# Kernel tuning notes

Hardware: AMD Instinct MI355X
Metric: run time of the kernel (lower is better)

Reference implementation:

```python
import jax, jax.numpy as jnp
import numpy as np

H = 8  # num_heads
EPS = 1e-6


def _pos_encoding(S, D):
    # absolute sinusoidal positional encoding, shape [S, D]
    pos = jnp.arange(S, dtype=jnp.float32)[:, None]
    div = jnp.exp(jnp.arange(0, D, 2, dtype=jnp.float32) * (-np.log(10000.0) / D))
    pe = jnp.zeros((S, D), dtype=jnp.float32)
    pe = pe.at[:, 0::2].set(jnp.sin(pos * div))
    pe = pe.at[:, 1::2].set(jnp.cos(pos * div))
    return pe


def setup_inputs() -> dict:
    key = jax.random.key(0)
    ks = jax.random.split(key, 5)
    S, B, D = 2048, 16, 1024
    s = 1.0 / np.sqrt(D)
    return {
        'x': jax.random.normal(ks[0], (S, B, D), dtype=jnp.float32),
        'Wq': jax.random.normal(ks[1], (D, D), dtype=jnp.float32) * s,
        'bq': jnp.zeros((D,), dtype=jnp.float32),
        'Wk': jax.random.normal(ks[2], (D, D), dtype=jnp.float32) * s,
        'bk': jnp.zeros((D,), dtype=jnp.float32),
        'Wv': jax.random.normal(ks[3], (D, D), dtype=jnp.float32) * s,
        'bv': jnp.zeros((D,), dtype=jnp.float32),
        'Wo': jax.random.normal(ks[4], (D, D), dtype=jnp.float32) * s,
        'bo': jnp.zeros((D,), dtype=jnp.float32),
    }


def reference(x, Wq, bq, Wk, bk, Wv, bv, Wo, bo):
    # x: [S, B, D]  (nn.Transformer layout)
    S, B, D = x.shape
    dh = D // H
    h = x + _pos_encoding(S, D)[:, None, :]
    # projections (torch Linear: y = x @ W.T + b), split into heads
    q = (h @ Wq.T + bq).reshape(S, B, H, dh)
    k = (h @ Wk.T + bk).reshape(S, B, H, dh)
    v = (h @ Wv.T + bv).reshape(S, B, H, dh)
    # kernel feature map phi(u) = elu(u) + 1 (Katharopoulos linear attention)
    pq = jax.nn.elu(q) + 1.0
    pk = jax.nn.elu(k) + 1.0
    # global (non-causal) linear attention:
    # kv state: sum_s phi(k_s) v_s^T  -> [B, H, dh, dh]
    kv = jnp.einsum('sbhd,sbhe->bhde', pk, v)
    # normalizer: sum_s phi(k_s)     -> [B, H, dh]
    z = pk.sum(axis=0)
    num = jnp.einsum('sbhd,bhde->sbhe', pq, kv)   # [S, B, H, dh]
    den = jnp.einsum('sbhd,bhd->sbh', pq, z)       # [S, B, H]
    att = num / (den[..., None] + EPS)
    out = att.reshape(S, B, D) @ Wo.T + bo
    return out
```

## Files before the change

kernel.cpp:

```cpp
#include <hip/hip_runtime.h>
#include <hip/hip_bf16.h>
#include <stdint.h>


typedef __bf16 bf16x8 __attribute__((ext_vector_type(8)));
typedef float f32x4 __attribute__((ext_vector_type(4)));

#define S_LEN 2048
#define B_SZ  16
#define D_MOD 1024
#define N_H   8
#define D_H   128

__device__ __forceinline__ short f2bf(float f) {
  __bf16 b = (__bf16)f;
  return __builtin_bit_cast(short, b);
}
__device__ __forceinline__ float bf2f(short s) {
  return (float)__builtin_bit_cast(__bf16, s);
}

__device__ __forceinline__ void gload_lds16(const short* g, short* l) {
  __builtin_amdgcn_global_load_lds(
      (__attribute__((address_space(1))) void*)(g),
      (__attribute__((address_space(3))) void*)(l), 16, 0, 0);
}

__device__ __forceinline__ int swz(int o) { return o ^ (((o >> 7) & 3) << 4); }

__device__ __forceinline__ bf16x8 ld_bf8_8al(const short* p) {
  union { unsigned long long u[2]; bf16x8 v; } x;
  x.u[0] = *(const unsigned long long*)p;
  x.u[1] = *(const unsigned long long*)(p + 4);
  return x.v;
}

__global__ void prep_h(const float* __restrict__ x, short* __restrict__ h) {
  size_t idx8 = (size_t)blockIdx.x * blockDim.x + threadIdx.x;
  size_t base = idx8 * 8;
  int d = (int)(base & 1023);
  int r = (int)(base >> 10);
  int s = r >> 4;
  float4 v0 = *(const float4*)(x + base);
  float4 v1 = *(const float4*)(x + base + 4);
  float vs[8] = {v0.x, v0.y, v0.z, v0.w, v1.x, v1.y, v1.z, v1.w};
  const float kdiv = -9.210340371976184f / 1024.0f;
  bf16x8 ov;
#pragma unroll
  for (int t = 0; t < 8; ++t) {
    int dc = d + t;
    float div = __expf((float)(dc & ~1) * kdiv);
    float ang = (float)s * div;
    float pe = (dc & 1) ? __cosf(ang) : __sinf(ang);
    ov[t] = (__bf16)(vs[t] + pe);
  }
  *(bf16x8*)(h + base) = ov;
}

__global__ void pack_w(const float* __restrict__ Wq, const float* __restrict__ Wk,
                       const float* __restrict__ Wv, const float* __restrict__ Wo,
                       short* __restrict__ Wcat) {
  size_t i4 = (size_t)blockIdx.x * blockDim.x + threadIdx.x;
  size_t base = i4 * 4;
  const float* src;
  size_t off;
  if (base < 1048576)      { src = Wq; off = base; }
  else if (base < 2097152) { src = Wk; off = base - 1048576; }
  else if (base < 3145728) { src = Wv; off = base - 2097152; }
  else                     { src = Wo; off = base - 3145728; }
  float4 v = *(const float4*)(src + off);
  alignas(8) short o[4] = {f2bf(v.x), f2bf(v.y), f2bf(v.z), f2bf(v.w)};
  *(uint2*)(Wcat + base) = *(const uint2*)o;
}

template <int K>
__device__ __forceinline__ void core_256(const short* __restrict__ A,
                                         const short* __restrict__ W,
                                         char* Lb, f32x4 (&acc)[8][4]) {
  constexpr int NT = K / 32;
  static_assert(NT >= 4, "pipeline needs K >= 128");
  const int tid = threadIdx.x;
  const int lane = tid & 63;
  const int wave = tid >> 6;
  const int wm = wave & 1, wn = wave >> 1;
  const int l15 = lane & 15, quad = lane >> 4;

  const int oA0 = tid * 16, oA1 = 8192 + tid * 16;
  const int lA0 = swz(oA0), lA1 = swz(oA1);
  const short* gA0 = A + (size_t)(lA0 >> 6) * K + ((lA0 & 63) >> 1);
  const short* gA1 = A + (size_t)((lA1 - 8192) >> 6) * K + 128 * K + (((lA1 - 8192) & 63) >> 1);
  const short* gW0 = W + (size_t)(lA0 >> 6) * K + ((lA0 & 63) >> 1);
  const short* gW1 = W + (size_t)((lA1 - 8192) >> 6) * K + 128 * K + (((lA1 - 8192) & 63) >> 1);

  int rA[8], rW[4];
#pragma unroll
  for (int i = 0; i < 8; ++i)
    rA[i] = swz((wm * 128 + i * 16 + l15) * 64 + quad * 16);
#pragma unroll
  for (int j = 0; j < 4; ++j)
    rW[j] = 16384 + swz((wn * 64 + j * 16 + l15) * 64 + quad * 16);

  auto stage = [&](int t) {
    char* sb = Lb + (t & 3) * 32768;
    const int k0 = t * 32;
    gload_lds16(gA0 + k0, (short*)(sb + oA0));
    gload_lds16(gA1 + k0, (short*)(sb + oA1));
    gload_lds16(gW0 + k0, (short*)(sb + 16384 + oA0));
    gload_lds16(gW1 + k0, (short*)(sb + 16384 + oA1));
  };
  auto step = [&](int t, bool do_stage) {
    char* cb = Lb + (t & 3) * 32768;
    bf16x8 af[8], wf[4];
#pragma unroll
    for (int i = 0; i < 8; ++i) af[i] = *(const bf16x8*)(cb + rA[i]);
#pragma unroll
    for (int j = 0; j < 4; ++j) wf[j] = *(const bf16x8*)(cb + rW[j]);
    if (do_stage) stage(t + 3);
    __builtin_amdgcn_s_setprio(1);
#pragma unroll
    for (int i = 0; i < 8; ++i)
#pragma unroll
      for (int j = 0; j < 4; ++j)
        acc[i][j] = __builtin_amdgcn_mfma_f32_16x16x32_bf16(af[i], wf[j], acc[i][j], 0, 0, 0);
    __builtin_amdgcn_s_setprio(0);
    asm volatile("s_waitcnt lgkmcnt(0)" ::: "memory");
    __builtin_amdgcn_sched_barrier(0);
  };

  stage(0); stage(1); stage(2);

  for (int t = 0; t <= NT - 4; ++t) {
    asm volatile("s_waitcnt vmcnt(8)" ::: "memory");
    __builtin_amdgcn_s_barrier();
    step(t, true);
  }
  asm volatile("s_waitcnt vmcnt(8)" ::: "memory");
  __builtin_amdgcn_s_barrier();
  step(NT - 3, false);
  asm volatile("s_waitcnt vmcnt(4)" ::: "memory");
  __builtin_amdgcn_s_barrier();
  step(NT - 2, false);
  asm volatile("s_waitcnt vmcnt(0)" ::: "memory");
  __builtin_amdgcn_s_barrier();
  step(NT - 1, false);
}

template <int K>
__device__ __forceinline__ void core_128(const short* __restrict__ A,
                                         const short* __restrict__ W,
                                         char* Lb, f32x4 (&acc)[4][4]) {
  constexpr int NT = K / 32;
  static_assert(NT >= 4, "pipeline needs K >= 128");
  const int tid = threadIdx.x;
  const int lane = tid & 63;
  const int wm = (tid >> 6) & 1, wn = tid >> 7;
  const int l15 = lane & 15, quad = lane >> 4;

  const int oA0 = tid * 16, oA1 = 4096 + tid * 16;
  const int lA0 = swz(oA0), lA1 = swz(oA1);
  const short* gA0 = A + (size_t)(lA0 >> 6) * K + ((lA0 & 63) >> 1);
  const short* gA1 = A + (size_t)((lA1 - 4096) >> 6) * K + 64 * K + (((lA1 - 4096) & 63) >> 1);
  const short* gW0 = W + (size_t)(lA0 >> 6) * K + ((lA0 & 63) >> 1);
  const short* gW1 = W + (size_t)((lA1 - 4096) >> 6) * K + 64 * K + (((lA1 - 4096) & 63) >> 1);

  int rA[4], rW[4];
#pragma unroll
  for (int i = 0; i < 4; ++i)
    rA[i] = swz((wm * 64 + i * 16 + l15) * 64 + quad * 16);
#pragma unroll
  for (int j = 0; j < 4; ++j)
    rW[j] = 8192 + swz((wn * 64 + j * 16 + l15) * 64 + quad * 16);

  auto stage = [&](int t) {
    char* sb = Lb + (t & 3) * 16384;
    const int k0 = t * 32;
    gload_lds16(gA0 + k0, (short*)(sb + oA0));
    gload_lds16(gA1 + k0, (short*)(sb + oA1));
    gload_lds16(gW0 + k0, (short*)(sb + 8192 + oA0));
    gload_lds16(gW1 + k0, (short*)(sb + 8192 + oA1));
  };
  auto step = [&](int t, bool do_stage) {
    char* cb = Lb + (t & 3) * 16384;
    bf16x8 af[4], wf[4];
#pragma unroll
    for (int i = 0; i < 4; ++i) af[i] = *(const bf16x8*)(cb + rA[i]);
#pragma unroll
    for (int j = 0; j < 4; ++j) wf[j] = *(const bf16x8*)(cb + rW[j]);
    if (do_stage) stage(t + 3);
    __builtin_amdgcn_s_setprio(1);
#pragma unroll
    for (int i = 0; i < 4; ++i)
#pragma unroll
      for (int j = 0; j < 4; ++j)
        acc[i][j] = __builtin_amdgcn_mfma_f32_16x16x32_bf16(af[i], wf[j], acc[i][j], 0, 0, 0);
    __builtin_amdgcn_s_setprio(0);
    asm volatile("s_waitcnt lgkmcnt(0)" ::: "memory");
    __builtin_amdgcn_sched_barrier(0);
  };

  stage(0); stage(1); stage(2);

  for (int t = 0; t <= NT - 4; ++t) {
    asm volatile("s_waitcnt vmcnt(8)" ::: "memory");
    __builtin_amdgcn_s_barrier();
    step(t, true);
  }
  asm volatile("s_waitcnt vmcnt(8)" ::: "memory");
  __builtin_amdgcn_s_barrier();
  step(NT - 3, false);
  asm volatile("s_waitcnt vmcnt(4)" ::: "memory");
  __builtin_amdgcn_s_barrier();
  step(NT - 2, false);
  asm volatile("s_waitcnt vmcnt(0)" ::: "memory");
  __builtin_amdgcn_s_barrier();
  step(NT - 1, false);
}

__launch_bounds__(512, 2)
__global__ void gemm_qkv(const short* __restrict__ h, const short* __restrict__ Wqkv,
                         const float* __restrict__ bq, const float* __restrict__ bk,
                         const float* __restrict__ bv,
                         short* __restrict__ pq, short* __restrict__ pk,
                         short* __restrict__ pv) {
  __shared__ alignas(16) char Lb[131072];
  const int lin = blockIdx.y * 12 + blockIdx.x;
  const int x = lin & 7, q = lin >> 3;
  const int xm = x >> 1, xn = x & 1;
  const int bm = xm * 32 + q / 6;
  const int bn = xn * 6 + q % 6;
  const int rowBase = bm * 256, colBase = bn * 256;

  f32x4 acc[8][4] = {};
  core_256<1024>(h + (size_t)rowBase * 1024, Wqkv + (size_t)colBase * 1024, Lb, acc);

  const int tid = threadIdx.x;
  const int lane = tid & 63;
  const int wave = tid >> 6;
  const int wm = wave & 1, wn = wave >> 1;
  const int l15 = lane & 15, quad = lane >> 4;

  const int p = bn >> 2;
  const float* bias = (p == 0) ? bq : (p == 1) ? bk : bv;
  short* Pout = (p == 0) ? pq : (p == 1) ? pk : pv;

  __syncthreads();
  short* Lt = (short*)Lb;
#pragma unroll
  for (int j = 0; j < 4; ++j) {
    const int c = wn * 64 + j * 16 + l15;
    const float bval = bias[(bn & 3) * 256 + c];
#pragma unroll
    for (int i = 0; i < 8; ++i) {
#pragma unroll
      for (int r = 0; r < 4; ++r) {
        const int mloc = wm * 128 + i * 16 + quad * 4 + r;
        float v = acc[i][j][r] + bval;
        if (p < 2) v = v > 0.f ? v + 1.f : __expf(v);
        Lt[mloc * 256 + (c ^ ((mloc & 7) << 3))] = f2bf(v);
      }
    }
  }
  __syncthreads();
  const int g16 = tid >> 4, L = tid & 15;
#pragma unroll
  for (int it = 0; it < 16; ++it) {
    const int chunk = it * 32 + g16;
    const int row = chunk >> 1, hhl = chunk & 1;
    const int grow = rowBase + row;
    const int s = grow >> 4, b = grow & 15;
    const int hh = (bn & 3) * 2 + hhl;
    const short* src = Lt + row * 256 + ((hhl * 128 + L * 8) ^ ((row & 7) << 3));
    short* dst = Pout + (((size_t)b * N_H + hh) * S_LEN + s) * D_H + L * 8;
    *(uint4*)dst = *(const uint4*)src;
  }
}

__launch_bounds__(256, 2)
__global__ void kv_kernel(const short* __restrict__ pk, const short* __restrict__ pv,
                          short* __restrict__ kvT, float* __restrict__ z) {
  __shared__ alignas(16) short Vt[128 * 44];
  __shared__ alignas(16) short Pt[128 * 44];
  __shared__ float zl[16 * 128];
  const int bh = blockIdx.x;
  const short* Vg = pv + (size_t)bh * S_LEN * D_H;
  const short* Pg = pk + (size_t)bh * S_LEN * D_H;

  const int tid = threadIdx.x;
  const int lane = tid & 63;
  const int wm = (tid >> 6) & 1, wn = tid >> 7;
  const int l15 = lane & 15, quad = lane >> 4;
  const int s_loc = tid >> 3, e8 = tid & 7;

  const short* vsrc = Vg + s_loc * 128 + e8 * 8;
  const short* psrc = Pg + s_loc * 128 + e8 * 8;

  f32x4 acc[4][4] = {};
  uint4 cv0, cv1, cp0, cp1;
  cv0 = *(const uint4*)(vsrc);
  cv1 = *(const uint4*)(vsrc + 64);
  cp0 = *(const uint4*)(psrc);
  cp1 = *(const uint4*)(psrc + 64);

  for (int t = 0; t < 64; ++t) {
    __builtin_amdgcn_s_barrier();
    const short* sv0 = (const short*)&cv0;
    const short* sv1 = (const short*)&cv1;
    const short* sp0 = (const short*)&cp0;
    const short* sp1 = (const short*)&cp1;
#pragma unroll
    for (int u = 0; u < 8; ++u) {
      Vt[(e8 * 8 + u) * 44 + s_loc] = sv0[u];
      Vt[(64 + e8 * 8 + u) * 44 + s_loc] = sv1[u];
      Pt[(e8 * 8 + u) * 44 + s_loc] = sp0[u];
      Pt[(64 + e8 * 8 + u) * 44 + s_loc] = sp1[u];
    }
    if (t < 63) {
      const int o = (t + 1) * 32 * 128;
      cv0 = *(const uint4*)(vsrc + o);
      cv1 = *(const uint4*)(vsrc + o + 64);
      cp0 = *(const uint4*)(psrc + o);
      cp1 = *(const uint4*)(psrc + o + 64);
    }
    asm volatile("s_waitcnt lgkmcnt(0)" ::: "memory");
    __builtin_amdgcn_sched_barrier(0);
    __builtin_amdgcn_s_barrier();
    bf16x8 af[4], wf[4];
#pragma unroll
    for (int i = 0; i < 4; ++i)
      af[i] = ld_bf8_8al(&Vt[(wm * 64 + i * 16 + l15) * 44 + quad * 8]);
#pragma unroll
    for (int j = 0; j < 4; ++j)
      wf[j] = ld_bf8_8al(&Pt[(wn * 64 + j * 16 + l15) * 44 + quad * 8]);
#pragma unroll
    for (int i = 0; i < 4; ++i)
#pragma unroll
      for (int j = 0; j < 4; ++j)
        acc[i][j] = __builtin_amdgcn_mfma_f32_16x16x32_bf16(af[i], wf[j], acc[i][j], 0, 0, 0);
    asm volatile("s_waitcnt lgkmcnt(0)" ::: "memory");
    __builtin_amdgcn_sched_barrier(0);
  }

#pragma unroll
  for (int j = 0; j < 4; ++j) {
    const int d = wn * 64 + j * 16 + l15;
#pragma unroll
    for (int i = 0; i < 4; ++i) {
#pragma unroll
      for (int r = 0; r < 4; ++r) {
        const int e = wm * 64 + i * 16 + quad * 4 + r;
        kvT[(size_t)bh * (D_H * D_H) + (size_t)e * D_H + d] = f2bf(acc[i][j][r]);
      }
    }
  }
  __syncthreads();
  {
    const int d8 = tid & 15, so = tid >> 4;
    float za[8] = {};
    for (int s = so; s < S_LEN; s += 16) {
      uint4 u = *(const uint4*)(Pg + (size_t)s * 128 + d8 * 8);
      const short* sp = (const short*)&u;
#pragma unroll
      for (int u2 = 0; u2 < 8; ++u2) za[u2] += bf2f(sp[u2]);
    }
#pragma unroll
    for (int u2 = 0; u2 < 8; ++u2) zl[so * 128 + d8 * 8 + u2] = za[u2];
  }
  __syncthreads();
  if (tid < 128) {
    float sum = 0.f;
#pragma unroll
    for (int k = 0; k < 16; ++k) sum += zl[k * 128 + tid];
    z[bh * D_H + tid] = sum;
  }
}

__launch_bounds__(256, 2)
__global__ void attn_kernel(const short* __restrict__ pq, const short* __restrict__ kvT,
                            const float* __restrict__ z, short* __restrict__ att) {
  __shared__ alignas(16) char Lb[65536];
  __shared__ float den_lds[128];
  __shared__ float z_lds[128];
  const int s0 = blockIdx.x * 128;
  const int bh = blockIdx.y;
  const int tid = threadIdx.x;

  const short* Abase = pq + ((size_t)bh * S_LEN + s0) * D_H;
  const short* Wbase = kvT + (size_t)bh * (D_H * D_H);

  f32x4 acc[4][4] = {};
  core_128<128>(Abase, Wbase, Lb, acc);

  if (tid < 128) z_lds[tid] = z[bh * D_H + tid];
  __syncthreads();
  if (tid < 128) {
    const short* prow = Abase + (size_t)tid * D_H;
    float sum = 0.f;
#pragma unroll
    for (int d = 0; d < D_H; d += 8) {
      bf16x8 vv = *(const bf16x8*)(prow + d);
#pragma unroll
      for (int t = 0; t < 8; ++t) sum += (float)vv[t] * z_lds[d + t];
    }
    den_lds[tid] = sum + 1e-6f;
  }
  __syncthreads();

  const int lane = tid & 63;
  const int wm = (tid >> 6) & 1, wn = tid >> 7;
  const int l15 = lane & 15, quad = lane >> 4;
  const int b = bh >> 3, hd = bh & 7;
#pragma unroll
  for (int j = 0; j < 4; ++j) {
    const int e = wn * 64 + j * 16 + l15;
#pragma unroll
    for (int i = 0; i < 4; ++i) {
#pragma unroll
      for (int r = 0; r < 4; ++r) {
        int mloc = wm * 64 + i * 16 + quad * 4 + r;
        float a = acc[i][j][r] / den_lds[mloc];
        att[((size_t)(s0 + mloc) * B_SZ + b) * D_MOD + hd * D_H + e] = f2bf(a);
      }
    }
  }
}

__launch_bounds__(512, 2)
__global__ void gemm_out(const short* __restrict__ att, const short* __restrict__ WoB,
                         const float* __restrict__ bo, float* __restrict__ out) {
  __shared__ alignas(16) char Lb[131072];
  const int lin = blockIdx.y * 4 + blockIdx.x;
  const int x = lin & 7, q = lin >> 3;
  const int bn = q & 3;
  const int bm = x * 16 + (q >> 2);
  const int rowBase = bm * 256, colBase = bn * 256;

  f32x4 acc[8][4] = {};
  core_256<1024>(att + (size_t)rowBase * 1024, WoB + (size_t)colBase * 1024, Lb, acc);

  const int tid = threadIdx.x;
  const int lane = tid & 63;
  const int wave = tid >> 6;
  const int wm = wave & 1, wn = wave >> 1;
  const int l15 = lane & 15, quad = lane >> 4;
#pragma unroll
  for (int j = 0; j < 4; ++j) {
    const int gcol = colBase + wn * 64 + j * 16 + l15;
    const float bval = bo[gcol];
#pragma unroll
    for (int i = 0; i < 8; ++i) {
#pragma unroll
      for (int r = 0; r < 4; ++r) {
        int grow = rowBase + wm * 128 + i * 16 + quad * 4 + r;
        out[(size_t)grow * 1024 + gcol] = acc[i][j][r] + bval;
      }
    }
  }
}

extern "C" void kernel_launch(void* const* d_in, const int* in_sizes, int n_in,
                              void* d_out, int out_size, void* d_ws, size_t ws_size,
                              hipStream_t stream) {
  const float* x  = (const float*)d_in[0];
  const float* Wq = (const float*)d_in[1];
  const float* bq = (const float*)d_in[2];
  const float* Wk = (const float*)d_in[3];
  const float* bk = (const float*)d_in[4];
  const float* Wv = (const float*)d_in[5];
  const float* bv = (const float*)d_in[6];
  const float* Wo = (const float*)d_in[7];
  const float* bo = (const float*)d_in[8];
  float* out = (float*)d_out;

  char* ws = (char*)d_ws;
  short* h    = (short*)(ws);
  short* Wcat = (short*)(ws + 67108864);
  short* pq   = (short*)(ws + 75497472);
  short* pk   = (short*)(ws + 142606336);
  short* pv   = (short*)(ws + 209715200);
  short* kvT  = (short*)(ws + 276824064);
  float* z    = (float*)(ws + 281018368);

  prep_h<<<16384, 256, 0, stream>>>(x, h);
  pack_w<<<4096, 256, 0, stream>>>(Wq, Wk, Wv, Wo, Wcat);
  gemm_qkv<<<dim3(12, 128), 512, 0, stream>>>(h, Wcat, bq, bk, bv, pq, pk, pv);
  kv_kernel<<<128, 256, 0, stream>>>(pk, pv, kvT, z);
  attn_kernel<<<dim3(16, 128), 256, 0, stream>>>(pq, kvT, z, h );
  gemm_out<<<dim3(4, 128), 512, 0, stream>>>(h, Wcat + 3145728, bo, out);
}
```

Baseline: 685.6 us.

## Restructure 256-tile GEMM pipeline with K=64 steps and split KV reduction

The 256x256 GEMM core now stages 64-wide K tiles in two LDS buffers, interleaving half-tile LDS reads, async global-to-LDS loads and MFMA groups with barriers between them. The goal is to hide load latency better and keep fewer fragments live in registers. Launch bounds for the two big GEMMs drop to one block per CU to match the full 128KB LDS use. The KV state computation is also split over four sequence chunks with fp32 partials plus a reduce kernel, so 512 blocks run instead of 128. In exchange this adds an extra kernel launch and fp32 partial traffic through the workspace.

After: 637.3 us. 7.0% less time.

```diff
diff --git a/kernel.cpp b/kernel.cpp
--- a/kernel.cpp
+++ b/kernel.cpp
@@ -77,72 +77,97 @@
 __device__ __forceinline__ void core_256(const short* __restrict__ A,
                                          const short* __restrict__ W,
                                          char* Lb, f32x4 (&acc)[8][4]) {
-  constexpr int NT = K / 32;
-  static_assert(NT >= 4, "pipeline needs K >= 128");
+  constexpr int NT = K / 64;
+  static_assert(NT >= 4 && (NT & 1) == 0, "K must be multiple of 128, >= 256");
   const int tid = threadIdx.x;
   const int lane = tid & 63;
   const int wave = tid >> 6;
   const int wm = wave & 1, wn = wave >> 1;
   const int l15 = lane & 15, quad = lane >> 4;
 
-  const int oA0 = tid * 16, oA1 = 8192 + tid * 16;
-  const int lA0 = swz(oA0), lA1 = swz(oA1);
-  const short* gA0 = A + (size_t)(lA0 >> 6) * K + ((lA0 & 63) >> 1);
-  const short* gA1 = A + (size_t)((lA1 - 8192) >> 6) * K + 128 * K + (((lA1 - 8192) & 63) >> 1);
-  const short* gW0 = W + (size_t)(lA0 >> 6) * K + ((lA0 & 63) >> 1);
-  const short* gW1 = W + (size_t)((lA1 - 8192) >> 6) * K + 128 * K + (((lA1 - 8192) & 63) >> 1);
-
-  int rA[8], rW[4];
+  const int o0 = tid * 16, o1 = 8192 + tid * 16;
+  const int r0s = o0 >> 6, r1s = o1 >> 6;
+  const int c0 = ((o0 & 63) ^ (((o0 >> 7) & 3) << 4)) >> 1;
+  const int c1 = ((o1 & 63) ^ (((o1 >> 7) & 3) << 4)) >> 1;
+  const short* gA0 = A + (size_t)r0s * K + c0;
+  const short* gA1 = A + (size_t)r1s * K + c1;
+  const short* gW0 = W + (size_t)r0s * K + c0;
+  const short* gW1 = W + (size_t)r1s * K + c1;
+
+  int rAo[8], rWo[4];
 #pragma unroll
   for (int i = 0; i < 8; ++i)
-    rA[i] = swz((wm * 128 + i * 16 + l15) * 64 + quad * 16);
+    rAo[i] = swz((wm * 128 + i * 16 + l15) * 64 + quad * 16);
 #pragma unroll
   for (int j = 0; j < 4; ++j)
-    rW[j] = 16384 + swz((wn * 64 + j * 16 + l15) * 64 + quad * 16);
-
-  auto stage = [&](int t) {
-    char* sb = Lb + (t & 3) * 32768;
-    const int k0 = t * 32;
-    gload_lds16(gA0 + k0, (short*)(sb + oA0));
-    gload_lds16(gA1 + k0, (short*)(sb + oA1));
-    gload_lds16(gW0 + k0, (short*)(sb + 16384 + oA0));
-    gload_lds16(gW1 + k0, (short*)(sb + 16384 + oA1));
+    rWo[j] = swz((wn * 64 + j * 16 + l15) * 64 + quad * 16);
+
+  bf16x8 af[4], wf[4];
+
+  auto stg = [&](int tau, int op, int kh) {
+    char* d = Lb + (tau & 1) * 65536 + op * 32768 + kh * 16384;
+    const int ko = tau * 64 + kh * 32;
+    const short* s0 = (op ? gW0 : gA0) + ko;
+    const short* s1 = (op ? gW1 : gA1) + ko;
+    gload_lds16(s0, (short*)(d + o0));
+    gload_lds16(s1, (short*)(d + o1));
   };
-  auto step = [&](int t, bool do_stage) {
-    char* cb = Lb + (t & 3) * 32768;
-    bf16x8 af[8], wf[4];
-#pragma unroll
-    for (int i = 0; i < 8; ++i) af[i] = *(const bf16x8*)(cb + rA[i]);
-#pragma unroll
-    for (int j = 0; j < 4; ++j) wf[j] = *(const bf16x8*)(cb + rW[j]);
-    if (do_stage) stage(t + 3);
-    __builtin_amdgcn_s_setprio(1);
-#pragma unroll
-    for (int i = 0; i < 8; ++i)
-#pragma unroll
-      for (int j = 0; j < 4; ++j)
-        acc[i][j] = __builtin_amdgcn_mfma_f32_16x16x32_bf16(af[i], wf[j], acc[i][j], 0, 0, 0);
-    __builtin_amdgcn_s_setprio(0);
+  auto rd0 = [&](int tau, int kh) {
+    char* base = Lb + (tau & 1) * 65536 + kh * 16384;
+#pragma unroll
+    for (int j = 0; j < 4; ++j) wf[j] = *(const bf16x8*)(base + 32768 + rWo[j]);
+#pragma unroll
+    for (int i = 0; i < 4; ++i) af[i] = *(const bf16x8*)(base + rAo[i]);
+  };
+  auto rd1 = [&](int tau, int kh) {
+    char* base = Lb + (tau & 1) * 65536 + kh * 16384;
+#pragma unroll
+    for (int i = 0; i < 4; ++i) af[i] = *(const bf16x8*)(base + rAo[4 + i]);
+  };
+  auto mm = [&](int ih) {
+    __builtin_amdgcn_s_barrier();
     asm volatile("s_waitcnt lgkmcnt(0)" ::: "memory");
     __builtin_amdgcn_sched_barrier(0);
+    __builtin_amdgcn_s_setprio(1);
+#pragma unroll
+    for (int i = 0; i < 4; ++i)
+#pragma unroll
+      for (int j = 0; j < 4; ++j)
+        acc[ih * 4 + i][j] =
+            __builtin_amdgcn_mfma_f32_16x16x32_bf16(af[i], wf[j], acc[ih * 4 + i][j], 0, 0, 0);
+    __builtin_amdgcn_s_setprio(0);
+    __builtin_amdgcn_s_barrier();
   };
 
-  stage(0); stage(1); stage(2);
-
-  for (int t = 0; t <= NT - 4; ++t) {
-    asm volatile("s_waitcnt vmcnt(8)" ::: "memory");
-    __builtin_amdgcn_s_barrier();
-    step(t, true);
-  }
-  asm volatile("s_waitcnt vmcnt(8)" ::: "memory");
+  stg(0, 1, 0); stg(0, 0, 0); stg(0, 1, 1); stg(0, 0, 1);
+  stg(1, 1, 0); stg(1, 0, 0); stg(1, 1, 1);
+  asm volatile("s_waitcnt vmcnt(6)" ::: "memory");
   __builtin_amdgcn_s_barrier();
-  step(NT - 3, false);
-  asm volatile("s_waitcnt vmcnt(4)" ::: "memory");
-  __builtin_amdgcn_s_barrier();
-  step(NT - 2, false);
-  asm volatile("s_waitcnt vmcnt(0)" ::: "memory");
-  __builtin_amdgcn_s_barrier();
-  step(NT - 1, false);
+
+  for (int t = 0; t + 3 < NT; t += 2) {
+    rd0(t, 0);     stg(t + 1, 0, 1);                                          mm(0);
+    rd1(t, 0);     stg(t + 2, 1, 0);                                          mm(1);
+    rd0(t, 1);     stg(t + 2, 0, 0);                                          mm(0);
+    rd1(t, 1);     stg(t + 2, 1, 1);
+    asm volatile("s_waitcnt vmcnt(6)" ::: "memory");                          mm(1);
+    rd0(t + 1, 0); stg(t + 2, 0, 1);                                          mm(0);
+    rd1(t + 1, 0); stg(t + 3, 1, 0);                                          mm(1);
+    rd0(t + 1, 1); stg(t + 3, 0, 0);                                          mm(0);
+    rd1(t + 1, 1); stg(t + 3, 1, 1);
+    asm volatile("s_waitcnt vmcnt(6)" ::: "memory");                          mm(1);
+  }
+  {
+    const int t = NT - 2;
+    rd0(t, 0);     stg(t + 1, 0, 1);                                          mm(0);
+    rd1(t, 0);                                                                mm(1);
+    rd0(t, 1);                                                                mm(0);
+    rd1(t, 1);
+    asm volatile("s_waitcnt vmcnt(0)" ::: "memory");                          mm(1);
+    rd0(t + 1, 0);                                                            mm(0);
+    rd1(t + 1, 0);                                                            mm(1);
+    rd0(t + 1, 1);                                                            mm(0);
+    rd1(t + 1, 1);                                                            mm(1);
+  }
 }
 
 template <int K>
@@ -216,7 +241,7 @@
   step(NT - 1, false);
 }
 
-__launch_bounds__(512, 2)
+__launch_bounds__(512, 1)
 __global__ void gemm_qkv(const short* __restrict__ h, const short* __restrict__ Wqkv,
                          const float* __restrict__ bq, const float* __restrict__ bk,
                          const float* __restrict__ bv,
@@ -276,14 +301,16 @@
 }
 
 __launch_bounds__(256, 2)
-__global__ void kv_kernel(const short* __restrict__ pk, const short* __restrict__ pv,
-                          short* __restrict__ kvT, float* __restrict__ z) {
+__global__ void kv_part(const short* __restrict__ pk, const short* __restrict__ pv,
+                        float* __restrict__ kvp, float* __restrict__ zp) {
   __shared__ alignas(16) short Vt[128 * 44];
   __shared__ alignas(16) short Pt[128 * 44];
   __shared__ float zl[16 * 128];
-  const int bh = blockIdx.x;
-  const short* Vg = pv + (size_t)bh * S_LEN * D_H;
-  const short* Pg = pk + (size_t)bh * S_LEN * D_H;
+  const int split = blockIdx.x;
+  const int bh = blockIdx.y;
+  const int sbase = split * 512;
+  const short* Vg = pv + ((size_t)bh * S_LEN + sbase) * D_H;
+  const short* Pg = pk + ((size_t)bh * S_LEN + sbase) * D_H;
 
   const int tid = threadIdx.x;
   const int lane = tid & 63;
@@ -301,7 +328,7 @@
   cp0 = *(const uint4*)(psrc);
   cp1 = *(const uint4*)(psrc + 64);
 
-  for (int t = 0; t < 64; ++t) {
+  for (int t = 0; t < 16; ++t) {
     __builtin_amdgcn_s_barrier();
     const short* sv0 = (const short*)&cv0;
     const short* sv1 = (const short*)&cv1;
@@ -314,7 +341,7 @@
       Pt[(e8 * 8 + u) * 44 + s_loc] = sp0[u];
       Pt[(64 + e8 * 8 + u) * 44 + s_loc] = sp1[u];
     }
-    if (t < 63) {
+    if (t < 15) {
       const int o = (t + 1) * 32 * 128;
       cv0 = *(const uint4*)(vsrc + o);
       cv1 = *(const uint4*)(vsrc + o + 64);
@@ -340,6 +367,7 @@
     __builtin_amdgcn_sched_barrier(0);
   }
 
+  float* kout = kvp + (size_t)(bh * 4 + split) * (D_H * D_H);
 #pragma unroll
   for (int j = 0; j < 4; ++j) {
     const int d = wn * 64 + j * 16 + l15;
@@ -348,7 +376,7 @@
 #pragma unroll
       for (int r = 0; r < 4; ++r) {
         const int e = wm * 64 + i * 16 + quad * 4 + r;
-        kvT[(size_t)bh * (D_H * D_H) + (size_t)e * D_H + d] = f2bf(acc[i][j][r]);
+        kout[(size_t)e * D_H + d] = acc[i][j][r];
       }
     }
   }
@@ -356,7 +384,7 @@
   {
     const int d8 = tid & 15, so = tid >> 4;
     float za[8] = {};
-    for (int s = so; s < S_LEN; s += 16) {
+    for (int s = so; s < 512; s += 16) {
       uint4 u = *(const uint4*)(Pg + (size_t)s * 128 + d8 * 8);
       const short* sp = (const short*)&u;
 #pragma unroll
@@ -370,7 +398,22 @@
     float sum = 0.f;
 #pragma unroll
     for (int k = 0; k < 16; ++k) sum += zl[k * 128 + tid];
-    z[bh * D_H + tid] = sum;
+    zp[(bh * 4 + split) * D_H + tid] = sum;
+  }
+}
+
+__global__ void kv_reduce(const float* __restrict__ kvp, const float* __restrict__ zp,
+                          short* __restrict__ kvT, float* __restrict__ z) {
+  const int bh = blockIdx.x;
+  const int tid = threadIdx.x;
+  const float* k0 = kvp + (size_t)(bh * 4) * (D_H * D_H);
+  for (int i = tid; i < D_H * D_H; i += 256) {
+    float s = k0[i] + k0[16384 + i] + k0[32768 + i] + k0[49152 + i];
+    kvT[(size_t)bh * (D_H * D_H) + i] = f2bf(s);
+  }
+  if (tid < 128) {
+    const float* z0 = zp + bh * 4 * D_H;
+    z[bh * D_H + tid] = z0[tid] + z0[D_H + tid] + z0[2 * D_H + tid] + z0[3 * D_H + tid];
   }
 }
 
@@ -424,7 +467,7 @@
   }
 }
 
-__launch_bounds__(512, 2)
+__launch_bounds__(512, 1)
 __global__ void gemm_out(const short* __restrict__ att, const short* __restrict__ WoB,
                          const float* __restrict__ bo, float* __restrict__ out) {
   __shared__ alignas(16) char Lb[131072];
@@ -479,11 +522,14 @@
   short* pv   = (short*)(ws + 209715200);
   short* kvT  = (short*)(ws + 276824064);
   float* z    = (float*)(ws + 281018368);
+  float* kvp  = (float*)(ws);
+  float* zp   = (float*)(ws + 33554432);
 
   prep_h<<<16384, 256, 0, stream>>>(x, h);
   pack_w<<<4096, 256, 0, stream>>>(Wq, Wk, Wv, Wo, Wcat);
   gemm_qkv<<<dim3(12, 128), 512, 0, stream>>>(h, Wcat, bq, bk, bv, pq, pk, pv);
-  kv_kernel<<<128, 256, 0, stream>>>(pk, pv, kvT, z);
+  kv_part<<<dim3(4, 128), 256, 0, stream>>>(pk, pv, kvp, zp);
+  kv_reduce<<<128, 256, 0, stream>>>(kvp, zp, kvT, z);
   attn_kernel<<<dim3(16, 128), 256, 0, stream>>>(pq, kvT, z, h );
   gemm_out<<<dim3(4, 128), 512, 0, stream>>>(h, Wcat + 3145728, bo, out);
 }
```
